# Optimization experiments

Hardware: AMD Instinct MI355X
Metric: run time of the kernel (lower is better)

The kernel has to match this reference:

```python
import jax, jax.numpy as jnp
import numpy as np

B, S, M, KD, VD, QD, H, NQ = 256, 200, 32, 128, 256, 128, 64, 10000
TA, TB, TC = 0.075, 0.088, 1.0  # triangular membership params a, b, c


def setup_inputs() -> dict:
    key = jax.random.key(0)
    ks = jax.random.split(key, 12)
    q_data = jax.random.randint(ks[0], (B, S), 0, NQ + 1)
    # kaiming-normal-ish embedding table; padding_idx=0 row zeroed
    q_embed_weight = jax.random.normal(ks[1], (NQ + 1, QD)) * np.sqrt(2.0 / QD)
    q_embed_weight = q_embed_weight.at[0].set(0.0)
    key_mem = jax.random.normal(ks[2], (M, KD)) * np.sqrt(2.0 / KD)
    value_mem = jax.random.normal(ks[3], (M, VD)) * np.sqrt(2.0 / VD)
    in_dim = VD + QD
    s = 1.0 / np.sqrt(H)
    W_ih = jax.random.uniform(ks[4], (4 * H, in_dim), minval=-s, maxval=s)
    W_hh = jax.random.uniform(ks[5], (4 * H, H), minval=-s, maxval=s)
    b_ih = jax.random.uniform(ks[6], (4 * H,), minval=-s, maxval=s)
    b_hh = jax.random.uniform(ks[7], (4 * H,), minval=-s, maxval=s)
    W_pred = jax.random.normal(ks[8], (1, H)) * np.sqrt(2.0 / H)
    b_pred = jnp.zeros((1,))
    init_h = jax.random.normal(ks[9], (B, H))
    init_c = jax.random.normal(ks[10], (B, H))
    return dict(q_data=q_data, q_embed_weight=q_embed_weight, key_mem=key_mem,
                value_mem=value_mem, W_ih=W_ih, W_hh=W_hh, b_ih=b_ih, b_hh=b_hh,
                W_pred=W_pred, b_pred=b_pred, init_h=init_h, init_c=init_c)


def triangular_layer(cw):
    """cw: [N, M] correlation weights -> [N] unique-row indices.
    Faithful to torch: trit-quantize each weight {0,1,2}, then map each row to its
    index in the (lexicographically sorted) unique-row table, which is exactly what
    the pairwise squared-distance matmul + (dist==0).nonzero() trick computes."""
    w = jnp.minimum((cw - TA) / (TB - TA), (TC - cw) / (TC - TB))
    w = jnp.maximum(w, 0.0)
    iv = jnp.where(w >= 0.6, 2, jnp.where(w >= 0.1, 1, 0)).astype(jnp.int32)  # [N, M]
    # pack 32 trits into two int32 keys (3^16 < 2^31)
    p = jnp.power(3, jnp.arange(16, dtype=jnp.int32))  # [16]
    kh = (iv[:, :16] * p).sum(1)
    kl = (iv[:, 16:] * p).sum(1)
    order = jnp.lexsort((kl, kh))  # primary key kh
    kh_s, kl_s = kh[order], kl[order]
    change = jnp.concatenate([jnp.zeros((1,), jnp.int32),
                              ((kh_s[1:] != kh_s[:-1]) | (kl_s[1:] != kl_s[:-1])).astype(jnp.int32)])
    rank_sorted = jnp.cumsum(change)
    inv = jnp.zeros(cw.shape[0], jnp.int32).at[order].set(rank_sorted)
    return inv


def reference(q_data, q_embed_weight, key_mem, value_mem, W_ih, W_hh, b_ih, b_hh,
              W_pred, b_pred, init_h, init_c):
    q_emb = q_embed_weight[q_data]                                  # [B,S,QD]
    cw = jax.nn.softmax(jnp.einsum('bsd,md->bsm', q_emb, key_mem))  # DKVMN attention
    read = jnp.einsum('bsm,mv->bsv', cw, value_mem)                 # [B,S,VD]
    ids = triangular_layer(cw.reshape(B * S, M))                    # [B*S]
    x = jnp.concatenate([read, q_emb], axis=-1)                     # [B,S,VD+QD]

    def step(carry, xt):
        h, c = carry
        g = xt @ W_ih.T + h @ W_hh.T + b_ih + b_hh
        i, f, gg, o = jnp.split(g, 4, axis=-1)
        c = jax.nn.sigmoid(f) * c + jax.nn.sigmoid(i) * jnp.tanh(gg)
        h = jax.nn.sigmoid(o) * jnp.tanh(c)
        return (h, c), h

    _, hs = jax.lax.scan(step, (init_h, init_c), jnp.swapaxes(x, 0, 1))
    hs = jnp.swapaxes(hs, 0, 1)                                     # [B,S,H]
    pred = jax.nn.sigmoid(hs @ W_pred.T + b_pred)[..., 0]           # [B,S]
    return pred, ids
```

## Files before the change

### kernel.cpp

```cpp
#include <hip/hip_runtime.h>

#define BB 256
#define SS 200
#define MM 32
#define KDIM 128
#define VDIM 256
#define QDIM 128
#define HH 64
#define NROWS 10001
#define NSAMP (BB*SS)
#define INDIM (VDIM+QDIM)
#define DHS 8192
#define DHMASK (DHS-1)
#define XR 16
#define CH 50
#define NB_ATTN 2501

typedef unsigned long long u64;
typedef unsigned int u32;

__device__ __forceinline__ float fexp(float x){ return __builtin_amdgcn_exp2f(x * 1.44269504f); }
__device__ __forceinline__ float fsigm(float x){ return __builtin_amdgcn_rcpf(1.f + fexp(-x)); }
__device__ __forceinline__ float ftanh(float x){ return 1.f - 2.f*__builtin_amdgcn_rcpf(1.f + fexp(2.f*x)); }
__device__ __forceinline__ int clampq(int q){ return q < 0 ? 0 : (q > NROWS-1 ? NROWS-1 : q); }

__device__ __forceinline__ u32 hash64(u64 x){
  x ^= x >> 33; x *= 0xff51afd7ed558ccdULL;
  x ^= x >> 33; x *= 0xc4ceb9fe1a85ec53ULL;
  x ^= x >> 33;
  return (u32)x;
}

__device__ __forceinline__ u64 shflx64(u64 v, int m){
  int lo = __shfl_xor((int)(u32)v, m, 64);
  int hi = __shfl_xor((int)(u32)(v >> 32), m, 64);
  return ((u64)(u32)hi << 32) | (u32)lo;
}

__global__ void k_tr(const float* __restrict__ W_ih, const float* __restrict__ key_mem,
                     float* __restrict__ WQT4, float* __restrict__ KT,
                     float* __restrict__ WVT, u32* __restrict__ present){
  int idx = blockIdx.x*256 + threadIdx.x;
  if (idx < 131072) {
    int dd = idx & 3, j = (idx >> 2) & 255, d4 = idx >> 10;
    WQT4[idx] = W_ih[j*INDIM + VDIM + 4*d4 + dd];
  } else if (idx < 135168) {
    int t = idx - 131072;
    int m = t & 31, d = t >> 5; KT[t] = key_mem[m*KDIM + d];
  } else if (idx < 200704) {
    int t = idx - 135168;
    int j = t & 255, v = t >> 8; WVT[v*256 + j] = W_ih[j*INDIM + v];
  } else {
    int t = idx - 200704;
    if (t < NROWS) present[t] = 0u;
  }
}

__global__ __launch_bounds__(256) void k_front(
    const float* __restrict__ emb, const float* __restrict__ KT,
    const float* __restrict__ val, const float* __restrict__ WVT,
    const int* __restrict__ q_data,
    float* __restrict__ CW, u64* __restrict__ KEYT,
    float* __restrict__ VW, u32* __restrict__ present){
  int bid = blockIdx.x;
  if (bid < NB_ATTN) {
    int w = threadIdx.x >> 6, l = threadIdx.x & 63;
    int n = bid*4 + w;
    __shared__ float se[4][QDIM];
    bool valid = (n < NROWS);
    if (valid) {
      se[w][l]      = emb[n*QDIM + l];
      se[w][l + 64] = emb[n*QDIM + l + 64];
    }
    __syncthreads();
    int m = l & 31;
    float logit = 0.f;
    if (valid && l < 32)
      for (int d = 0; d < KDIM; ++d) logit += se[w][d] * KT[d*32 + m];
    float mx = logit;
    #pragma unroll
    for (int msk = 16; msk >= 1; msk >>= 1) mx = fmaxf(mx, __shfl_xor(mx, msk, 64));
    float e = (l < 32) ? expf(logit - mx) : 0.f;
    float sum = e;
    #pragma unroll
    for (int msk = 16; msk >= 1; msk >>= 1) sum += __shfl_xor(sum, msk, 64);
    float cw = e / sum;
    float wv = fminf((cw - 0.075f)/0.013f, (1.0f - cw)/0.912f);
    wv = fmaxf(wv, 0.f);
    int iv = (wv >= 0.6f) ? 2 : ((wv >= 0.1f) ? 1 : 0);
    int ee = (m < 16) ? m + 16 : m - 16;
    u64 p3 = 1;
    for (int i = 0; i < 31; ++i) if (i < ee) p3 *= 3ULL;
    u64 term = (valid && l < 32) ? (u64)iv * p3 : 0ULL;
    #pragma unroll
    for (int msk = 16; msk >= 1; msk >>= 1) term += shflx64(term, msk);
    if (valid && l < 32) CW[n*256 + m] = cw;
    if (valid && l == 0) KEYT[n] = term;
  } else if (bid < NB_ATTN + MM) {
    int m = bid - NB_ATTN, j = threadIdx.x;
    __shared__ float sval[VDIM];
    sval[j] = val[m*VDIM + j];
    __syncthreads();
    float a0=0.f, a1=0.f, a2=0.f, a3=0.f;
    for (int v = 0; v < VDIM; v += 4) {
      a0 += sval[v+0]*WVT[(v+0)*256 + j];
      a1 += sval[v+1]*WVT[(v+1)*256 + j];
      a2 += sval[v+2]*WVT[(v+2)*256 + j];
      a3 += sval[v+3]*WVT[(v+3)*256 + j];
    }
    VW[m*256 + j] = (a0+a1)+(a2+a3);
  } else {
    int i = (bid - NB_ATTN - MM)*256 + threadIdx.x;
    if (i < NSAMP) present[clampq(q_data[i])] = 1u;
  }
}

__global__ __launch_bounds__(256) void k_xw(
    const float* __restrict__ CW, const float* __restrict__ emb,
    const float* __restrict__ VW, const float* __restrict__ WQT4,
    const float* __restrict__ b_ih, const float* __restrict__ b_hh,
    float* __restrict__ XW4){
  int base = blockIdx.x * XR;
  int j = threadIdx.x;
  __shared__ float scw[XR][32];
  __shared__ __align__(16) float ses[XR][QDIM];
  for (int idx = j; idx < XR*32; idx += 256) {
    int r = idx >> 5, m = idx & 31, n = base + r;
    scw[r][m] = (n < NROWS) ? CW[n*256 + m] : 0.f;
  }
  for (int idx = j; idx < XR*QDIM; idx += 256) {
    int r = idx >> 7, d = idx & 127, n = base + r;
    ses[r][d] = (n < NROWS) ? emb[n*QDIM + d] : 0.f;
  }
  __syncthreads();
  float bias = b_ih[j] + b_hh[j];
  float acc[XR];
  #pragma unroll
  for (int r = 0; r < XR; ++r) acc[r] = bias;
  for (int m = 0; m < MM; ++m) {
    float wv = VW[m*256 + j];
    #pragma unroll
    for (int r = 0; r < XR; ++r) acc[r] += scw[r][m] * wv;
  }
  for (int d4 = 0; d4 < QDIM/4; ++d4) {
    float4 wq = *(const float4*)(WQT4 + d4*1024 + j*4);
    #pragma unroll
    for (int r = 0; r < XR; ++r) {
      float4 ev = *(const float4*)(&ses[r][4*d4]);
      acc[r] += ev.x*wq.x + ev.y*wq.y + ev.z*wq.z + ev.w*wq.w;
    }
  }
  int gate = j >> 6, unit = j & 63;
  #pragma unroll
  for (int r = 0; r < XR; ++r)
    if (base + r < NROWS) XW4[(size_t)(base + r)*256 + 4*unit + gate] = acc[r];
}

__global__ __launch_bounds__(1024) void k_dedup(
    const u32* __restrict__ present, const u64* __restrict__ KEYT,
    u32* __restrict__ g_htab, u32* __restrict__ g_pay,
    u32* __restrict__ counter, u64* __restrict__ uniq){
  __shared__ u32 sh_tab[DHS];
  __shared__ u32 sh_pay[DHS];
  __shared__ u32 sh_cnt;
  int tid = threadIdx.x;
  for (int i = tid; i < DHS; i += 1024) sh_tab[i] = 0u;
  if (tid == 0) sh_cnt = 0u;
  __syncthreads();
  for (int n = tid; n < NROWS; n += 1024) {
    if (present[n] != 1u) continue;
    u64 key = KEYT[n];
    u32 h = hash64(key) & DHMASK;
    while (true) {
      u32 cur = sh_tab[h];
      if (cur != 0u) {
        if (KEYT[cur-1u] == key) break;
        h = (h + 1) & DHMASK; continue;
      }
      u32 prev = atomicCAS(&sh_tab[h], 0u, (u32)(n + 1));
      if (prev == 0u) {
        u32 idx = atomicAdd(&sh_cnt, 1u);
        uniq[idx] = key;
        sh_pay[h] = idx;
        break;
      }
      if (KEYT[prev-1u] == key) break;
      h = (h + 1) & DHMASK;
    }
  }
  __syncthreads();
  for (int i = tid; i < DHS; i += 1024) {
    u32 v = sh_tab[i];
    g_htab[i] = v;
    g_pay[i]  = v ? sh_pay[i] : 0u;
  }
  if (tid == 0) *counter = sh_cnt;
}

__global__ __launch_bounds__(256) void k_rank(const u64* __restrict__ uniq,
                                              const u32* __restrict__ counter,
                                              u32* __restrict__ RANK){
  __shared__ u64 chunk[2048];
  u32 U = *counter;
  int u = blockIdx.x*256 + threadIdx.x;
  u64 mykey = (u < (int)U) ? uniq[u] : 0;
  u32 cnt = 0;
  for (u32 base = 0; base < U; base += 2048) {
    u32 n = (U - base < 2048u) ? (U - base) : 2048u;
    __syncthreads();
    for (u32 t = threadIdx.x; t < n; t += 256) chunk[t] = uniq[base + t];
    __syncthreads();
    if (u < (int)U)
      for (u32 j = 0; j < n; ++j) cnt += (chunk[j] < mykey) ? 1u : 0u;
  }
  if (u < (int)U) RANK[u] = cnt;
}

__global__ void k_qrank(const u32* __restrict__ present, const u64* __restrict__ KEYT,
                        const u32* __restrict__ g_htab, const u32* __restrict__ g_pay,
                        const u32* __restrict__ RANK, u32* __restrict__ RANKQ){
  int n = blockIdx.x*blockDim.x + threadIdx.x;
  if (n >= NROWS || present[n] != 1u) return;
  u64 key = KEYT[n];
  u32 h = hash64(key) & DHMASK;
  while (true) {
    u32 cur = g_htab[h];
    if (cur != 0u && KEYT[cur-1u] == key) { RANKQ[n] = RANK[g_pay[h]]; return; }
    h = (h + 1) & DHMASK;
  }
}

__global__ void k_ids(const int* __restrict__ q_data, const u32* __restrict__ RANKQ,
                      float* __restrict__ out_ids){
  int i = blockIdx.x*blockDim.x + threadIdx.x;
  if (i >= NSAMP) return;
  out_ids[i] = (float)RANKQ[clampq(q_data[i])];
}

__global__ __launch_bounds__(256, 1) void k_lstm(
    const int* __restrict__ q_data, const float* __restrict__ XW4,
    const float* __restrict__ W_hh,
    const float* __restrict__ W_pred, const float* __restrict__ b_pred,
    const float* __restrict__ init_h, const float* __restrict__ init_c,
    float* __restrict__ out_pred){
  const int b = blockIdx.x, t = threadIdx.x;
  const int w = t >> 6, l = t & 63;
  const int g = l >> 4, u = l & 15;
  const int unit = w*16 + u;
  __shared__ float XWc[CH][256];
  __shared__ __align__(16) float Hbuf[SS][68];
  __shared__ float swp[HH];
  __shared__ int   sq[SS];
  for (int s = t; s < SS; s += 256) sq[s] = clampq(q_data[b*SS + s]);
  if (t < HH) swp[t] = W_pred[t];

  float wgt[HH];
  {
    const float4* wr = (const float4*)(W_hh + (size_t)(g*HH + unit)*HH);
    #pragma unroll
    for (int j4 = 0; j4 < HH/4; ++j4) {
      float4 v = wr[j4];
      wgt[4*j4+0]=v.x; wgt[4*j4+1]=v.y; wgt[4*j4+2]=v.z; wgt[4*j4+3]=v.w;
    }
  }
  float hfull[HH];
  {
    const float4* ih = (const float4*)(init_h + b*HH);
    #pragma unroll
    for (int j4 = 0; j4 < HH/4; ++j4) {
      float4 v = ih[j4];
      hfull[4*j4+0]=v.x; hfull[4*j4+1]=v.y; hfull[4*j4+2]=v.z; hfull[4*j4+3]=v.w;
    }
  }
  float c  = init_c[b*HH + unit];
  float bp = b_pred[0];
  __syncthreads();

  for (int cs = 0; cs < SS; cs += CH) {
    for (int rr = w; rr < CH; rr += 4) {
      float4 xv = *(const float4*)(XW4 + (size_t)sq[cs + rr]*256 + 4*l);
      int wp = l >> 4, up = l & 15;
      XWc[rr][wp*64 +  0 + up] = xv.x;
      XWc[rr][wp*64 + 16 + up] = xv.y;
      XWc[rr][wp*64 + 32 + up] = xv.z;
      XWc[rr][wp*64 + 48 + up] = xv.w;
    }
    __syncthreads();
    for (int sl = 0; sl < CH; ++sl) {
      const int s = cs + sl;
      float a0=0.f, a1=0.f, a2=0.f, a3=0.f;
      #pragma unroll
      for (int j = 0; j < 16; ++j) {
        a0 += wgt[j   ]*hfull[j   ];
        a1 += wgt[j+16]*hfull[j+16];
        a2 += wgt[j+32]*hfull[j+32];
        a3 += wgt[j+48]*hfull[j+48];
      }
      float a = XWc[sl][w*64 + l] + ((a0+a1)+(a2+a3));
      float v0 = a;
      float v1 = __shfl_xor(a, 16, 64);
      float v2 = __shfl_xor(a, 32, 64);
      float v3 = __shfl_xor(v1, 32, 64);
      float vv[4] = {v0, v1, v2, v3};
      float ii = vv[g], ff = vv[g^1], gg = vv[g^2], oo = vv[g^3];
      c = fsigm(ff)*c + fsigm(ii)*ftanh(gg);
      float hh = fsigm(oo)*ftanh(c);
      if (g == 0) Hbuf[s][unit] = hh;
      __syncthreads();
      const float4* hb = (const float4*)(&Hbuf[s][0]);
      #pragma unroll
      for (int j4 = 0; j4 < HH/4; ++j4) {
        float4 v = hb[j4];
        hfull[4*j4+0]=v.x; hfull[4*j4+1]=v.y; hfull[4*j4+2]=v.z; hfull[4*j4+3]=v.w;
      }
    }
  }
  __syncthreads();
  if (t < SS) {
    float acc = 0.f;
    #pragma unroll 16
    for (int kk = 0; kk < HH; ++kk) {
      int k2 = (kk + t) & 63;
      acc += Hbuf[t][k2] * swp[k2];
    }
    out_pred[b*SS + t] = fsigm(acc + bp);
  }
}

extern "C" void kernel_launch(void* const* d_in, const int* in_sizes, int n_in,
                              void* d_out, int out_size, void* d_ws, size_t ws_size,
                              hipStream_t stream) {
  const int*   q_data  = (const int*)d_in[0];
  const float* emb     = (const float*)d_in[1];
  const float* keym    = (const float*)d_in[2];
  const float* val     = (const float*)d_in[3];
  const float* W_ih    = (const float*)d_in[4];
  const float* W_hh    = (const float*)d_in[5];
  const float* b_ih    = (const float*)d_in[6];
  const float* b_hh    = (const float*)d_in[7];
  const float* W_pred  = (const float*)d_in[8];
  const float* b_pred  = (const float*)d_in[9];
  const float* init_h  = (const float*)d_in[10];
  const float* init_c  = (const float*)d_in[11];

  char* ws = (char*)d_ws;
  float* XW4     = (float*)(ws + 0);
  float* VW      = (float*)(ws + 10241024);
  u64*  KEYT     = (u64*) (ws + 10273792);
  u64*  uniq     = (u64*) (ws + 10353920);
  u32*  RANK     = (u32*) (ws + 10434048);
  u32*  g_htab   = (u32*) (ws + 10474240);
  u32*  g_pay    = (u32*) (ws + 10507008);
  u32*  counter  = (u32*) (ws + 10539776);
  u32*  present  = (u32*) (ws + 10539840);
  u32*  RANKQ    = (u32*) (ws + 10579904);
  float* WQT4    = (float*)(ws + 10619968);
  float* KT      = (float*)(ws + 11144256);
  float* WVT     = (float*)(ws + 11160640);
  float* CW      = XW4;

  float* out_pred = (float*)d_out;
  float* out_ids  = out_pred + NSAMP;

  hipLaunchKernelGGL(k_tr,    dim3(824), dim3(256), 0, stream,
                     W_ih, keym, WQT4, KT, WVT, present);
  hipLaunchKernelGGL(k_front, dim3(NB_ATTN + MM + 200), dim3(256), 0, stream,
                     emb, KT, val, WVT, q_data, CW, KEYT, VW, present);
  hipLaunchKernelGGL(k_dedup, dim3(1), dim3(1024), 0, stream,
                     present, KEYT, g_htab, g_pay, counter, uniq);
  hipLaunchKernelGGL(k_rank,  dim3((NROWS+255)/256), dim3(256), 0, stream, uniq, counter, RANK);
  hipLaunchKernelGGL(k_qrank, dim3((NROWS+255)/256), dim3(256), 0, stream,
                     present, KEYT, g_htab, g_pay, RANK, RANKQ);
  hipLaunchKernelGGL(k_xw,    dim3((NROWS+XR-1)/XR), dim3(256), 0, stream,
                     CW, emb, VW, WQT4, b_ih, b_hh, XW4);
  hipLaunchKernelGGL(k_ids,   dim3((NSAMP+255)/256), dim3(256), 0, stream, q_data, RANKQ, out_ids);
  hipLaunchKernelGGL(k_lstm,  dim3(BB), dim3(256), 0, stream,
                     q_data, XW4, W_hh, W_pred, b_pred, init_h, init_c, out_pred);
}
```

Before: 276.1 us.

## Fuse dedup, rank and query-rank kernels; pack two sequences per LSTM block

Merges the hash dedup, rank counting and per-question rank lookup into one single-block kernel that keeps the hash table in shared memory. This drops two launches and the global hash-table round trip. The cost is that the O(U^2) rank count now runs on only 1024 threads. The LSTM kernel now runs two batch rows per 512-thread block with a smaller XW chunk, halving the grid to 128 blocks. The attention logit dot product is split across both halves of each wavefront so all 64 lanes do work.

```diff
diff --git a/kernel.cpp b/kernel.cpp
--- a/kernel.cpp
+++ b/kernel.cpp
@@ -13,7 +13,7 @@
 #define DHS 8192
 #define DHMASK (DHS-1)
 #define XR 16
-#define CH 50
+#define CH2 20
 #define NB_ATTN 2501
 
 typedef unsigned long long u64;
@@ -73,10 +73,11 @@
       se[w][l + 64] = emb[n*QDIM + l + 64];
     }
     __syncthreads();
-    int m = l & 31;
-    float logit = 0.f;
-    if (valid && l < 32)
-      for (int d = 0; d < KDIM; ++d) logit += se[w][d] * KT[d*32 + m];
+    int m = l & 31, half = l >> 5;
+    float part = 0.f;
+    if (valid)
+      for (int d = 0; d < 64; ++d) part += se[w][half*64 + d] * KT[(half*64 + d)*32 + m];
+    float logit = part + __shfl_xor(part, 32, 64);
     float mx = logit;
     #pragma unroll
     for (int msk = 16; msk >= 1; msk >>= 1) mx = fmaxf(mx, __shfl_xor(mx, msk, 64));
@@ -115,51 +116,9 @@
   }
 }
 
-__global__ __launch_bounds__(256) void k_xw(
-    const float* __restrict__ CW, const float* __restrict__ emb,
-    const float* __restrict__ VW, const float* __restrict__ WQT4,
-    const float* __restrict__ b_ih, const float* __restrict__ b_hh,
-    float* __restrict__ XW4){
-  int base = blockIdx.x * XR;
-  int j = threadIdx.x;
-  __shared__ float scw[XR][32];
-  __shared__ __align__(16) float ses[XR][QDIM];
-  for (int idx = j; idx < XR*32; idx += 256) {
-    int r = idx >> 5, m = idx & 31, n = base + r;
-    scw[r][m] = (n < NROWS) ? CW[n*256 + m] : 0.f;
-  }
-  for (int idx = j; idx < XR*QDIM; idx += 256) {
-    int r = idx >> 7, d = idx & 127, n = base + r;
-    ses[r][d] = (n < NROWS) ? emb[n*QDIM + d] : 0.f;
-  }
-  __syncthreads();
-  float bias = b_ih[j] + b_hh[j];
-  float acc[XR];
-  #pragma unroll
-  for (int r = 0; r < XR; ++r) acc[r] = bias;
-  for (int m = 0; m < MM; ++m) {
-    float wv = VW[m*256 + j];
-    #pragma unroll
-    for (int r = 0; r < XR; ++r) acc[r] += scw[r][m] * wv;
-  }
-  for (int d4 = 0; d4 < QDIM/4; ++d4) {
-    float4 wq = *(const float4*)(WQT4 + d4*1024 + j*4);
-    #pragma unroll
-    for (int r = 0; r < XR; ++r) {
-      float4 ev = *(const float4*)(&ses[r][4*d4]);
-      acc[r] += ev.x*wq.x + ev.y*wq.y + ev.z*wq.z + ev.w*wq.w;
-    }
-  }
-  int gate = j >> 6, unit = j & 63;
-  #pragma unroll
-  for (int r = 0; r < XR; ++r)
-    if (base + r < NROWS) XW4[(size_t)(base + r)*256 + 4*unit + gate] = acc[r];
-}
-
-__global__ __launch_bounds__(1024) void k_dedup(
+__global__ __launch_bounds__(1024) void k_dedup2(
     const u32* __restrict__ present, const u64* __restrict__ KEYT,
-    u32* __restrict__ g_htab, u32* __restrict__ g_pay,
-    u32* __restrict__ counter, u64* __restrict__ uniq){
+    u64* __restrict__ uniq, u32* __restrict__ RANK, u32* __restrict__ RANKQ){
   __shared__ u32 sh_tab[DHS];
   __shared__ u32 sh_pay[DHS];
   __shared__ u32 sh_cnt;
@@ -188,46 +147,68 @@
       h = (h + 1) & DHMASK;
     }
   }
-  __syncthreads();
-  for (int i = tid; i < DHS; i += 1024) {
-    u32 v = sh_tab[i];
-    g_htab[i] = v;
-    g_pay[i]  = v ? sh_pay[i] : 0u;
-  }
-  if (tid == 0) *counter = sh_cnt;
-}
-
-__global__ __launch_bounds__(256) void k_rank(const u64* __restrict__ uniq,
-                                              const u32* __restrict__ counter,
-                                              u32* __restrict__ RANK){
-  __shared__ u64 chunk[2048];
-  u32 U = *counter;
-  int u = blockIdx.x*256 + threadIdx.x;
-  u64 mykey = (u < (int)U) ? uniq[u] : 0;
-  u32 cnt = 0;
-  for (u32 base = 0; base < U; base += 2048) {
-    u32 n = (U - base < 2048u) ? (U - base) : 2048u;
-    __syncthreads();
-    for (u32 t = threadIdx.x; t < n; t += 256) chunk[t] = uniq[base + t];
-    __syncthreads();
-    if (u < (int)U)
-      for (u32 j = 0; j < n; ++j) cnt += (chunk[j] < mykey) ? 1u : 0u;
-  }
-  if (u < (int)U) RANK[u] = cnt;
-}
-
-__global__ void k_qrank(const u32* __restrict__ present, const u64* __restrict__ KEYT,
-                        const u32* __restrict__ g_htab, const u32* __restrict__ g_pay,
-                        const u32* __restrict__ RANK, u32* __restrict__ RANKQ){
-  int n = blockIdx.x*blockDim.x + threadIdx.x;
-  if (n >= NROWS || present[n] != 1u) return;
-  u64 key = KEYT[n];
-  u32 h = hash64(key) & DHMASK;
-  while (true) {
-    u32 cur = g_htab[h];
-    if (cur != 0u && KEYT[cur-1u] == key) { RANKQ[n] = RANK[g_pay[h]]; return; }
-    h = (h + 1) & DHMASK;
-  }
+  __threadfence();
+  __syncthreads();
+  u32 U = sh_cnt;
+  for (int u = tid; u < (int)U; u += 1024) {
+    u64 k = uniq[u];
+    u32 cnt = 0;
+    for (u32 j = 0; j < U; ++j) cnt += (uniq[j] < k) ? 1u : 0u;
+    RANK[u] = cnt;
+  }
+  __threadfence();
+  __syncthreads();
+  for (int n = tid; n < NROWS; n += 1024) {
+    if (present[n] != 1u) continue;
+    u64 key = KEYT[n];
+    u32 h = hash64(key) & DHMASK;
+    while (true) {
+      u32 cur = sh_tab[h];
+      if (cur != 0u && KEYT[cur-1u] == key) { RANKQ[n] = RANK[sh_pay[h]]; break; }
+      h = (h + 1) & DHMASK;
+    }
+  }
+}
+
+__global__ __launch_bounds__(256) void k_xw(
+    const float* __restrict__ CW, const float* __restrict__ emb,
+    const float* __restrict__ VW, const float* __restrict__ WQT4,
+    const float* __restrict__ b_ih, const float* __restrict__ b_hh,
+    float* __restrict__ XW4){
+  int base = blockIdx.x * XR;
+  int j = threadIdx.x;
+  __shared__ float scw[XR][32];
+  __shared__ __align__(16) float ses[XR][QDIM];
+  for (int idx = j; idx < XR*32; idx += 256) {
+    int r = idx >> 5, m = idx & 31, n = base + r;
+    scw[r][m] = (n < NROWS) ? CW[n*256 + m] : 0.f;
+  }
+  for (int idx = j; idx < XR*QDIM; idx += 256) {
+    int r = idx >> 7, d = idx & 127, n = base + r;
+    ses[r][d] = (n < NROWS) ? emb[n*QDIM + d] : 0.f;
+  }
+  __syncthreads();
+  float bias = b_ih[j] + b_hh[j];
+  float acc[XR];
+  #pragma unroll
+  for (int r = 0; r < XR; ++r) acc[r] = bias;
+  for (int m = 0; m < MM; ++m) {
+    float wv = VW[m*256 + j];
+    #pragma unroll
+    for (int r = 0; r < XR; ++r) acc[r] += scw[r][m] * wv;
+  }
+  for (int d4 = 0; d4 < QDIM/4; ++d4) {
+    float4 wq = *(const float4*)(WQT4 + d4*1024 + j*4);
+    #pragma unroll
+    for (int r = 0; r < XR; ++r) {
+      float4 ev = *(const float4*)(&ses[r][4*d4]);
+      acc[r] += ev.x*wq.x + ev.y*wq.y + ev.z*wq.z + ev.w*wq.w;
+    }
+  }
+  int gate = j >> 6, unit = j & 63;
+  #pragma unroll
+  for (int r = 0; r < XR; ++r)
+    if (base + r < NROWS) XW4[(size_t)(base + r)*256 + 4*unit + gate] = acc[r];
 }
 
 __global__ void k_ids(const int* __restrict__ q_data, const u32* __restrict__ RANKQ,
@@ -237,21 +218,23 @@
   out_ids[i] = (float)RANKQ[clampq(q_data[i])];
 }
 
-__global__ __launch_bounds__(256, 1) void k_lstm(
+__global__ __launch_bounds__(512, 1) void k_lstm(
     const int* __restrict__ q_data, const float* __restrict__ XW4,
     const float* __restrict__ W_hh,
     const float* __restrict__ W_pred, const float* __restrict__ b_pred,
     const float* __restrict__ init_h, const float* __restrict__ init_c,
     float* __restrict__ out_pred){
-  const int b = blockIdx.x, t = threadIdx.x;
-  const int w = t >> 6, l = t & 63;
+  const int t = threadIdx.x;
+  const int e = t >> 8, tl = t & 255;
+  const int w = tl >> 6, l = t & 63;
   const int g = l >> 4, u = l & 15;
   const int unit = w*16 + u;
-  __shared__ float XWc[CH][256];
-  __shared__ __align__(16) float Hbuf[SS][68];
+  const int b = blockIdx.x*2 + e;
+  __shared__ float XWc[2][CH2][256];
+  __shared__ __align__(16) float Hbuf[2][SS][68];
   __shared__ float swp[HH];
-  __shared__ int   sq[SS];
-  for (int s = t; s < SS; s += 256) sq[s] = clampq(q_data[b*SS + s]);
+  __shared__ int   sq[2][SS];
+  for (int s = tl; s < SS; s += 256) sq[e][s] = clampq(q_data[b*SS + s]);
   if (t < HH) swp[t] = W_pred[t];
 
   float wgt[HH];
@@ -276,17 +259,17 @@
   float bp = b_pred[0];
   __syncthreads();
 
-  for (int cs = 0; cs < SS; cs += CH) {
-    for (int rr = w; rr < CH; rr += 4) {
-      float4 xv = *(const float4*)(XW4 + (size_t)sq[cs + rr]*256 + 4*l);
+  for (int cs = 0; cs < SS; cs += CH2) {
+    for (int rr = w; rr < CH2; rr += 4) {
+      float4 xv = *(const float4*)(XW4 + (size_t)sq[e][cs + rr]*256 + 4*l);
       int wp = l >> 4, up = l & 15;
-      XWc[rr][wp*64 +  0 + up] = xv.x;
-      XWc[rr][wp*64 + 16 + up] = xv.y;
-      XWc[rr][wp*64 + 32 + up] = xv.z;
-      XWc[rr][wp*64 + 48 + up] = xv.w;
+      XWc[e][rr][wp*64 +  0 + up] = xv.x;
+      XWc[e][rr][wp*64 + 16 + up] = xv.y;
+      XWc[e][rr][wp*64 + 32 + up] = xv.z;
+      XWc[e][rr][wp*64 + 48 + up] = xv.w;
     }
     __syncthreads();
-    for (int sl = 0; sl < CH; ++sl) {
+    for (int sl = 0; sl < CH2; ++sl) {
       const int s = cs + sl;
       float a0=0.f, a1=0.f, a2=0.f, a3=0.f;
       #pragma unroll
@@ -296,18 +279,17 @@
         a2 += wgt[j+32]*hfull[j+32];
         a3 += wgt[j+48]*hfull[j+48];
       }
-      float a = XWc[sl][w*64 + l] + ((a0+a1)+(a2+a3));
-      float v0 = a;
+      float a = XWc[e][sl][w*64 + l] + ((a0+a1)+(a2+a3));
       float v1 = __shfl_xor(a, 16, 64);
       float v2 = __shfl_xor(a, 32, 64);
       float v3 = __shfl_xor(v1, 32, 64);
-      float vv[4] = {v0, v1, v2, v3};
+      float vv[4] = {a, v1, v2, v3};
       float ii = vv[g], ff = vv[g^1], gg = vv[g^2], oo = vv[g^3];
       c = fsigm(ff)*c + fsigm(ii)*ftanh(gg);
       float hh = fsigm(oo)*ftanh(c);
-      if (g == 0) Hbuf[s][unit] = hh;
+      if (g == 0) Hbuf[e][s][unit] = hh;
       __syncthreads();
-      const float4* hb = (const float4*)(&Hbuf[s][0]);
+      const float4* hb = (const float4*)(&Hbuf[e][s][0]);
       #pragma unroll
       for (int j4 = 0; j4 < HH/4; ++j4) {
         float4 v = hb[j4];
@@ -316,14 +298,14 @@
     }
   }
   __syncthreads();
-  if (t < SS) {
+  if (tl < SS) {
     float acc = 0.f;
     #pragma unroll 16
     for (int kk = 0; kk < HH; ++kk) {
-      int k2 = (kk + t) & 63;
-      acc += Hbuf[t][k2] * swp[k2];
-    }
-    out_pred[b*SS + t] = fsigm(acc + bp);
+      int k2 = (kk + tl) & 63;
+      acc += Hbuf[e][tl][k2] * swp[k2];
+    }
+    out_pred[b*SS + tl] = fsigm(acc + bp);
   }
 }
 
@@ -349,9 +331,6 @@
   u64*  KEYT     = (u64*) (ws + 10273792);
   u64*  uniq     = (u64*) (ws + 10353920);
   u32*  RANK     = (u32*) (ws + 10434048);
-  u32*  g_htab   = (u32*) (ws + 10474240);
-  u32*  g_pay    = (u32*) (ws + 10507008);
-  u32*  counter  = (u32*) (ws + 10539776);
   u32*  present  = (u32*) (ws + 10539840);
   u32*  RANKQ    = (u32*) (ws + 10579904);
   float* WQT4    = (float*)(ws + 10619968);
@@ -362,18 +341,16 @@
   float* out_pred = (float*)d_out;
   float* out_ids  = out_pred + NSAMP;
 
-  hipLaunchKernelGGL(k_tr,    dim3(824), dim3(256), 0, stream,
+  hipLaunchKernelGGL(k_tr,     dim3(824), dim3(256), 0, stream,
                      W_ih, keym, WQT4, KT, WVT, present);
-  hipLaunchKernelGGL(k_front, dim3(NB_ATTN + MM + 200), dim3(256), 0, stream,
+  hipLaunchKernelGGL(k_front,  dim3(NB_ATTN + MM + 200), dim3(256), 0, stream,
                      emb, KT, val, WVT, q_data, CW, KEYT, VW, present);
-  hipLaunchKernelGGL(k_dedup, dim3(1), dim3(1024), 0, stream,
-                     present, KEYT, g_htab, g_pay, counter, uniq);
-  hipLaunchKernelGGL(k_rank,  dim3((NROWS+255)/256), dim3(256), 0, stream, uniq, counter, RANK);
-  hipLaunchKernelGGL(k_qrank, dim3((NROWS+255)/256), dim3(256), 0, stream,
-                     present, KEYT, g_htab, g_pay, RANK, RANKQ);
-  hipLaunchKernelGGL(k_xw,    dim3((NROWS+XR-1)/XR), dim3(256), 0, stream,
+  hipLaunchKernelGGL(k_dedup2, dim3(1), dim3(1024), 0, stream,
+                     present, KEYT, uniq, RANK, RANKQ);
+  hipLaunchKernelGGL(k_xw,     dim3((NROWS+XR-1)/XR), dim3(256), 0, stream,
                      CW, emb, VW, WQT4, b_ih, b_hh, XW4);
-  hipLaunchKernelGGL(k_ids,   dim3((NSAMP+255)/256), dim3(256), 0, stream, q_data, RANKQ, out_ids);
-  hipLaunchKernelGGL(k_lstm,  dim3(BB), dim3(256), 0, stream,
+  hipLaunchKernelGGL(k_ids,    dim3((NSAMP+255)/256), dim3(256), 0, stream,
+                     q_data, RANKQ, out_ids);
+  hipLaunchKernelGGL(k_lstm,   dim3(BB/2), dim3(512), 0, stream,
                      q_data, XW4, W_hh, W_pred, b_pred, init_h, init_c, out_pred);
 }
```

Measured after the change: 329.5 us. 19.4% more time.
